# Optimization experiments

Hardware: AMD Instinct MI355X
Metric: run time of the kernel (lower is better)

## Reference

```python
import jax, jax.numpy as jnp
import numpy as np

EMBED = 1024
HEADS = 16
HEAD_DIM = EMBED // HEADS


def setup_inputs() -> dict:
    key = jax.random.key(0)
    ks = jax.random.split(key, 8)
    N, S = 4, 2048
    scale = 1.0 / np.sqrt(HEAD_DIM)
    return {
        "values": jax.random.normal(ks[0], (N, S, EMBED), jnp.float32),
        "keys": jax.random.normal(ks[1], (N, S, EMBED), jnp.float32),
        "query": jax.random.normal(ks[2], (N, S, EMBED), jnp.float32),
        "Wv": jax.random.normal(ks[3], (HEAD_DIM, HEAD_DIM), jnp.float32) * scale,
        "Wk": jax.random.normal(ks[4], (HEAD_DIM, HEAD_DIM), jnp.float32) * scale,
        "Wq": jax.random.normal(ks[5], (HEAD_DIM, HEAD_DIM), jnp.float32) * scale,
        "Wo": jax.random.normal(ks[6], (EMBED, EMBED), jnp.float32) / np.sqrt(EMBED),
        "bo": jax.random.normal(ks[7], (EMBED,), jnp.float32) * 0.01,
    }


def reference(values, keys, query, Wv, Wk, Wq, Wo, bo):
    N = query.shape[0]
    # reshape to [N, S, H, D]
    v = values.reshape(N, -1, HEADS, HEAD_DIM)
    k = keys.reshape(N, -1, HEADS, HEAD_DIM)
    q = query.reshape(N, -1, HEADS, HEAD_DIM)
    # per-head linear projections (torch Linear: x @ W.T)
    v = jnp.einsum("nshd,ed->nshe", v, Wv)
    k = jnp.einsum("nshd,ed->nshe", k, Wk)
    q = jnp.einsum("nshd,ed->nshe", q, Wq)
    # full attention matrix [N, H, Q, K]; note scale uses embed_size**0.5 as in source
    energy = jnp.einsum("nqhd,nkhd->nhqk", q, k)
    attn = jax.nn.softmax(energy / jnp.sqrt(jnp.asarray(EMBED, energy.dtype)), axis=3)
    out = jnp.einsum("nhql,nlhd->nqhd", attn, v).reshape(N, -1, EMBED)
    return out @ Wo.T + bo
```

## Files before the change

### kernel.cpp

```cpp
#include <hip/hip_runtime.h>
#include <hip/hip_bf16.h>

#define EMBED 1024
#define HEADS 16
#define HD    64
#define NB    4
#define SEQ   2048

typedef __bf16 bf16x2 __attribute__((ext_vector_type(2)));
typedef __bf16 bf16x8 __attribute__((ext_vector_type(8)));
typedef float  f32x4  __attribute__((ext_vector_type(4)));
typedef float  f32x16 __attribute__((ext_vector_type(16)));

__device__ __forceinline__ unsigned short f2bf(float f) {
    union { float f; unsigned u; } v; v.f = f;
    unsigned r = v.u + 0x7fffu + ((v.u >> 16) & 1u);
    return (unsigned short)(r >> 16);
}
__device__ __forceinline__ unsigned pack2(float a, float b) {
#if __has_builtin(__builtin_amdgcn_cvt_pk_bf16_f32)
    union { bf16x2 v; unsigned u; } c;
    c.v = __builtin_amdgcn_cvt_pk_bf16_f32(a, b);
    return c.u;
#else
    return (unsigned)f2bf(a) | ((unsigned)f2bf(b) << 16);
#endif
}

__global__ __launch_bounds__(256) void cvt_kernel(const float* __restrict__ src,
                                                  unsigned* __restrict__ dst) {
    int i = blockIdx.x * 256 + threadIdx.x;
    float4 v = ((const float4*)src)[i];
    uint2 o;
    o.x = pack2(v.x, v.y);
    o.y = pack2(v.z, v.w);
    ((uint2*)dst)[i] = o;
}

__global__ __launch_bounds__(256) void proj_kernel(
    const float* __restrict__ xq, const float* __restrict__ xk, const float* __restrict__ xv,
    const float* __restrict__ Wq, const float* __restrict__ Wk, const float* __restrict__ Wv,
    unsigned short* __restrict__ Qp, unsigned short* __restrict__ Kp, unsigned short* __restrict__ Vt)
{
    __shared__ __align__(16) unsigned short Wl[64 * 72];
    __shared__ __align__(16) unsigned short Xl[256 * 72];

    int bx = blockIdx.x;
    int p  = bx >> 9;
    int r  = bx & 511;
    int st = r & 7, h = (r >> 3) & 15, n = r >> 7;
    int s0 = st * 256;

    const float* x = (p == 0) ? xq : (p == 1) ? xk : xv;
    const float* W = (p == 0) ? Wq : (p == 1) ? Wk : Wv;
    const float sc = (p == 0) ? 0.045084220027780106f : 1.0f;

    int tid = threadIdx.x;

    for (int i = 0; i < 4; ++i) {
        int idx = tid + i * 256;
        int row = idx >> 4, c4 = idx & 15;
        float4 wv = ((const float4*)W)[row * 16 + c4];
        uint2 pw;
        pw.x = pack2(wv.x, wv.y);
        pw.y = pack2(wv.z, wv.w);
        *(uint2*)&Wl[row * 72 + c4 * 4] = pw;
    }
    const float* xbase = x + (size_t)(n * SEQ + s0) * EMBED + h * HD;
    for (int i = 0; i < 16; ++i) {
        int idx = tid + i * 256;
        int row = idx >> 4, c4 = idx & 15;
        float4 v = *(const float4*)(xbase + (size_t)row * EMBED + c4 * 4);
        uint2 px;
        px.x = pack2(v.x, v.y);
        px.y = pack2(v.z, v.w);
        *(uint2*)&Xl[row * 72 + c4 * 4] = px;
    }
    __syncthreads();

    int w = tid >> 6, lane = tid & 63, ln = lane & 15, qd = lane >> 4;

    bf16x8 a[4][2], b[4][2];
#pragma unroll
    for (int mt = 0; mt < 4; ++mt)
#pragma unroll
        for (int kt = 0; kt < 2; ++kt)
            a[mt][kt] = *(const bf16x8*)&Xl[(w * 64 + mt * 16 + ln) * 72 + kt * 32 + qd * 8];
#pragma unroll
    for (int i = 0; i < 4; ++i)
#pragma unroll
        for (int kt = 0; kt < 2; ++kt)
            b[i][kt] = *(const bf16x8*)&Wl[(i * 16 + ln) * 72 + kt * 32 + qd * 8];

    f32x4 acc[4][4];
    const f32x4 fz = {0.f, 0.f, 0.f, 0.f};
#pragma unroll
    for (int i = 0; i < 4; ++i)
#pragma unroll
        for (int j = 0; j < 4; ++j) acc[i][j] = fz;

    if (p < 2) {
#pragma unroll
        for (int i = 0; i < 4; ++i)
#pragma unroll
            for (int j = 0; j < 4; ++j) {
                acc[i][j] = __builtin_amdgcn_mfma_f32_16x16x32_bf16(b[i][0], a[j][0], acc[i][j], 0, 0, 0);
                acc[i][j] = __builtin_amdgcn_mfma_f32_16x16x32_bf16(b[i][1], a[j][1], acc[i][j], 0, 0, 0);
            }
#pragma unroll
        for (int i = 0; i < 4; ++i)
#pragma unroll
            for (int j = 0; j < 4; ++j) {
                uint2 pk;
                pk.x = pack2(acc[i][j][0] * sc, acc[i][j][1] * sc);
                pk.y = pack2(acc[i][j][2] * sc, acc[i][j][3] * sc);
                *(uint2*)&Xl[(w * 64 + j * 16 + ln) * 72 + i * 16 + qd * 4] = pk;
            }
        __syncthreads();
        unsigned short* outp = (p == 0 ? Qp : Kp) + (size_t)(n * HEADS + h) * SEQ * HD + (size_t)s0 * HD;
        for (int i = 0; i < 8; ++i) {
            int idx = tid + i * 256;
            int row = idx >> 3, ch = idx & 7;
            *(uint4*)(outp + (size_t)row * HD + ch * 8) = *(const uint4*)&Xl[row * 72 + ch * 8];
        }
    } else {
#pragma unroll
        for (int mt = 0; mt < 4; ++mt)
#pragma unroll
            for (int i = 0; i < 4; ++i) {
                acc[mt][i] = __builtin_amdgcn_mfma_f32_16x16x32_bf16(a[mt][0], b[i][0], acc[mt][i], 0, 0, 0);
                acc[mt][i] = __builtin_amdgcn_mfma_f32_16x16x32_bf16(a[mt][1], b[i][1], acc[mt][i], 0, 0, 0);
            }
        __syncthreads();
#pragma unroll
        for (int mt = 0; mt < 4; ++mt)
#pragma unroll
            for (int i = 0; i < 4; ++i) {
                uint2 pk;
                pk.x = pack2(acc[mt][i][0], acc[mt][i][1]);
                pk.y = pack2(acc[mt][i][2], acc[mt][i][3]);
                *(uint2*)&Xl[(i * 16 + ln) * 264 + w * 64 + mt * 16 + qd * 4] = pk;
            }
        __syncthreads();
        unsigned short* outp = Vt + (size_t)(n * HEADS + h) * HD * SEQ + s0;
        for (int i = 0; i < 8; ++i) {
            int idx = tid + i * 256;
            int row = idx >> 5, ch = idx & 31;
            *(uint4*)(outp + (size_t)row * SEQ + ch * 8) = *(const uint4*)&Xl[row * 264 + ch * 8];
        }
    }
}

__global__ __launch_bounds__(512, 4) void attn_kernel(
    const unsigned short* __restrict__ Qp, const unsigned short* __restrict__ Kp,
    const unsigned short* __restrict__ Vt, unsigned short* __restrict__ Xattn)
{
    __shared__ __align__(16) unsigned short SMEM[18432];
    unsigned short* Kl = SMEM;
    unsigned short* Vl = SMEM + 9216;

    int bx = blockIdx.x;
    int head = bx >> 3, qt = bx & 7;
    int n = head >> 4, h16 = head & 15;
    int q0 = qt * 256;

    int tid = threadIdx.x;
    int w = tid >> 6, lane = tid & 63;
    int qc = lane & 31, hh = lane >> 5;

    const unsigned short* Qb = Qp + (size_t)head * SEQ * HD;
    const unsigned short* Kb = Kp + (size_t)head * SEQ * HD;
    const unsigned short* Vb = Vt + (size_t)head * HD * SEQ;

    bf16x8 qb[4];
    {
        int qrow = q0 + w * 32 + qc;
#pragma unroll
        for (int kk = 0; kk < 4; ++kk)
            qb[kk] = *(const bf16x8*)(Qb + (size_t)qrow * HD + kk * 16 + hh * 8);
    }

    f32x16 ot0, ot1;
#pragma unroll
    for (int i = 0; i < 16; ++i) { ot0[i] = 0.f; ot1[i] = 0.f; }
    float lsum = 0.f;

    int srow = tid >> 3, sch = tid & 7;

    uint4 rK, rV;
    rK = *(const uint4*)(Kb + (size_t)srow * HD + sch * 8);
    rV = *(const uint4*)(Vb + (size_t)srow * SEQ + 0 + sch * 8);
    *(uint4*)&Kl[srow * 72 + sch * 8] = rK;
    *(uint4*)&Vl[srow * 72 + sch * 8] = rV;
    rK = *(const uint4*)(Kb + (size_t)(64 + srow) * HD + sch * 8);
    rV = *(const uint4*)(Vb + (size_t)srow * SEQ + 64 + sch * 8);

    for (int kc = 0; kc < SEQ; kc += 64) {
        int cur = (kc >> 6) & 1, nxt = cur ^ 1;
        int curo = cur * 4608;
        __syncthreads();

        if (kc + 64 < SEQ) {
            *(uint4*)&Kl[nxt * 4608 + srow * 72 + sch * 8] = rK;
            *(uint4*)&Vl[nxt * 4608 + srow * 72 + sch * 8] = rV;
            int kn = kc + 128 <= SEQ - 64 ? kc + 128 : SEQ - 64;
            rK = *(const uint4*)(Kb + (size_t)(kn + srow) * HD + sch * 8);
            rV = *(const uint4*)(Vb + (size_t)srow * SEQ + kn + sch * 8);
        }

        unsigned pk[2][8];
#pragma unroll
        for (int kt = 0; kt < 2; ++kt) {
            f32x16 c;
#pragma unroll
            for (int i = 0; i < 16; ++i) c[i] = 0.f;
#pragma unroll
            for (int kk = 0; kk < 4; ++kk) {
                bf16x8 ka = *(const bf16x8*)&Kl[curo + (kt * 32 + qc) * 72 + kk * 16 + hh * 8];
                c = __builtin_amdgcn_mfma_f32_32x32x16_bf16(ka, qb[kk], c, 0, 0, 0);
            }
#pragma unroll
            for (int i = 0; i < 8; ++i) {
                float p0 = __builtin_amdgcn_exp2f(c[2 * i]);
                float p1 = __builtin_amdgcn_exp2f(c[2 * i + 1]);
                lsum += p0 + p1;
                pk[kt][i] = pack2(p0, p1);
            }
        }

#pragma unroll
        for (int g = 0; g < 4; ++g) {
            const unsigned* P = pk[g >> 1];
            int base = (g & 1) * 4;
            unsigned s0 = hh ? P[base + 0] : P[base + 2];
            unsigned s1 = hh ? P[base + 1] : P[base + 3];
            unsigned r0 = (unsigned)__shfl_xor((int)s0, 32);
            unsigned r1 = (unsigned)__shfl_xor((int)s1, 32);
            union { unsigned u[4]; bf16x8 v; } bb;
            bb.u[0] = hh ? r0 : P[base + 0];
            bb.u[1] = hh ? r1 : P[base + 1];
            bb.u[2] = hh ? P[base + 2] : r0;
            bb.u[3] = hh ? P[base + 3] : r1;
            bf16x8 va0 = *(const bf16x8*)&Vl[curo + qc * 72 + g * 16 + hh * 8];
            bf16x8 va1 = *(const bf16x8*)&Vl[curo + (32 + qc) * 72 + g * 16 + hh * 8];
            ot0 = __builtin_amdgcn_mfma_f32_32x32x16_bf16(va0, bb.v, ot0, 0, 0, 0);
            ot1 = __builtin_amdgcn_mfma_f32_32x32x16_bf16(va1, bb.v, ot1, 0, 0, 0);
        }
    }

    lsum += __shfl_xor(lsum, 32);
    float inv = 1.0f / lsum;

    __syncthreads();
    int qlocal = w * 32 + qc;
#pragma unroll
    for (int dt = 0; dt < 2; ++dt) {
        const f32x16& o = dt ? ot1 : ot0;
#pragma unroll
        for (int g = 0; g < 4; ++g) {
            uint2 p;
            p.x = pack2(o[4 * g + 0] * inv, o[4 * g + 1] * inv);
            p.y = pack2(o[4 * g + 2] * inv, o[4 * g + 3] * inv);
            *(uint2*)&SMEM[qlocal * 72 + dt * 32 + g * 8 + hh * 4] = p;
        }
    }
    __syncthreads();
    unsigned short* ob = Xattn + (size_t)(n * SEQ + q0) * EMBED + h16 * HD;
#pragma unroll
    for (int i = 0; i < 4; ++i) {
        int idx = tid + i * 512;
        int row = idx >> 3, ch = idx & 7;
        *(uint4*)(ob + (size_t)row * EMBED + ch * 8) = *(const uint4*)&SMEM[row * 72 + ch * 8];
    }
}

__global__ __launch_bounds__(256) void outproj_kernel(
    const unsigned short* __restrict__ X, const unsigned short* __restrict__ Wb,
    const float* __restrict__ bo, float* __restrict__ out)
{
    __shared__ __align__(16) unsigned short Al[128 * 72];
    __shared__ __align__(16) unsigned short Bl[128 * 72];

    int bx = blockIdx.x;
    int cm = bx >> 3, cn = bx & 7;
    int m0 = cm * 128, c0 = cn * 128;
    int tid = threadIdx.x;
    int w = tid >> 6, lane = tid & 63, ln = lane & 15, qd = lane >> 4;
    int rh = (w & 1) * 64, chh = (w >> 1) * 64;

    f32x4 acc[4][4];
    const f32x4 fz = {0.f, 0.f, 0.f, 0.f};
#pragma unroll
    for (int mt = 0; mt < 4; ++mt)
#pragma unroll
        for (int nt = 0; nt < 4; ++nt) acc[mt][nt] = fz;

    for (int k0 = 0; k0 < EMBED; k0 += 64) {
        for (int i = 0; i < 4; ++i) {
            int idx = tid + i * 256;
            int row = idx >> 3, ch = idx & 7;
            uint4 av = *(const uint4*)(X  + (size_t)(m0 + row) * EMBED + k0 + ch * 8);
            uint4 bv = *(const uint4*)(Wb + (size_t)(c0 + row) * EMBED + k0 + ch * 8);
            *(uint4*)&Al[row * 72 + ch * 8] = av;
            *(uint4*)&Bl[row * 72 + ch * 8] = bv;
        }
        __syncthreads();
        bf16x8 af[4][2], bf_[4][2];
#pragma unroll
        for (int mt = 0; mt < 4; ++mt)
#pragma unroll
            for (int kt = 0; kt < 2; ++kt)
                af[mt][kt] = *(const bf16x8*)&Al[(rh + mt * 16 + ln) * 72 + kt * 32 + qd * 8];
#pragma unroll
        for (int nt = 0; nt < 4; ++nt)
#pragma unroll
            for (int kt = 0; kt < 2; ++kt)
                bf_[nt][kt] = *(const bf16x8*)&Bl[(chh + nt * 16 + ln) * 72 + kt * 32 + qd * 8];
#pragma unroll
        for (int mt = 0; mt < 4; ++mt)
#pragma unroll
            for (int nt = 0; nt < 4; ++nt) {
                acc[mt][nt] = __builtin_amdgcn_mfma_f32_16x16x32_bf16(af[mt][0], bf_[nt][0], acc[mt][nt], 0, 0, 0);
                acc[mt][nt] = __builtin_amdgcn_mfma_f32_16x16x32_bf16(af[mt][1], bf_[nt][1], acc[mt][nt], 0, 0, 0);
            }
        __syncthreads();
    }

#pragma unroll
    for (int nt = 0; nt < 4; ++nt) {
        int col = c0 + chh + nt * 16 + ln;
        float bias = bo[col];
#pragma unroll
        for (int mt = 0; mt < 4; ++mt) {
            int row = m0 + rh + mt * 16 + qd * 4;
#pragma unroll
            for (int rg = 0; rg < 4; ++rg)
                out[(size_t)(row + rg) * EMBED + col] = acc[mt][nt][rg] + bias;
        }
    }
}

extern "C" void kernel_launch(void* const* d_in, const int* in_sizes, int n_in,
                              void* d_out, int out_size, void* d_ws, size_t ws_size,
                              hipStream_t stream) {
    const float* values = (const float*)d_in[0];
    const float* keys   = (const float*)d_in[1];
    const float* query  = (const float*)d_in[2];
    const float* Wv     = (const float*)d_in[3];
    const float* Wk     = (const float*)d_in[4];
    const float* Wq     = (const float*)d_in[5];
    const float* Wo     = (const float*)d_in[6];
    const float* bo     = (const float*)d_in[7];
    float* out = (float*)d_out;

    unsigned short* ws = (unsigned short*)d_ws;
    const size_t HSZ = (size_t)NB * HEADS * SEQ * HD;
    unsigned short* Qp = ws;
    unsigned short* Kp = Qp + HSZ;
    unsigned short* Vt = Kp + HSZ;
    unsigned short* Xa = Vt + HSZ;
    unsigned short* Wb = Xa + HSZ;

    cvt_kernel<<<1024, 256, 0, stream>>>(Wo, (unsigned*)Wb);
    proj_kernel<<<1536, 256, 0, stream>>>(query, keys, values, Wq, Wk, Wv, Qp, Kp, Vt);
    attn_kernel<<<512, 512, 0, stream>>>(Qp, Kp, Vt, Xa);
    outproj_kernel<<<512, 256, 0, stream>>>(Xa, Wb, bo, out);
}
```

Baseline: 276.5 us.

## Prefetch output-projection tiles into registers and use permlane32 swap in attention

```diff
diff --git a/kernel.cpp b/kernel.cpp
--- a/kernel.cpp
+++ b/kernel.cpp
@@ -11,6 +11,7 @@
 typedef __bf16 bf16x8 __attribute__((ext_vector_type(8)));
 typedef float  f32x4  __attribute__((ext_vector_type(4)));
 typedef float  f32x16 __attribute__((ext_vector_type(16)));
+typedef unsigned uint2v __attribute__((ext_vector_type(2)));
 
 __device__ __forceinline__ unsigned short f2bf(float f) {
     union { float f; unsigned u; } v; v.f = f;
@@ -183,7 +184,7 @@
     f32x16 ot0, ot1;
 #pragma unroll
     for (int i = 0; i < 16; ++i) { ot0[i] = 0.f; ot1[i] = 0.f; }
-    float lsum = 0.f;
+    float ls[4] = {0.f, 0.f, 0.f, 0.f};
 
     int srow = tid >> 3, sch = tid & 7;
 
@@ -223,7 +224,7 @@
             for (int i = 0; i < 8; ++i) {
                 float p0 = __builtin_amdgcn_exp2f(c[2 * i]);
                 float p1 = __builtin_amdgcn_exp2f(c[2 * i + 1]);
-                lsum += p0 + p1;
+                ls[i & 3] += p0 + p1;
                 pk[kt][i] = pack2(p0, p1);
             }
         }
@@ -232,15 +233,24 @@
         for (int g = 0; g < 4; ++g) {
             const unsigned* P = pk[g >> 1];
             int base = (g & 1) * 4;
+            union { unsigned u[4]; bf16x8 v; } bb;
+#if __has_builtin(__builtin_amdgcn_permlane32_swap)
+            uint2v r  = __builtin_amdgcn_permlane32_swap(P[base + 0], P[base + 2], false, false);
+            uint2v rr = __builtin_amdgcn_permlane32_swap(P[base + 1], P[base + 3], false, false);
+            bb.u[0] = r.x;
+            bb.u[1] = rr.x;
+            bb.u[2] = r.y;
+            bb.u[3] = rr.y;
+#else
             unsigned s0 = hh ? P[base + 0] : P[base + 2];
             unsigned s1 = hh ? P[base + 1] : P[base + 3];
             unsigned r0 = (unsigned)__shfl_xor((int)s0, 32);
             unsigned r1 = (unsigned)__shfl_xor((int)s1, 32);
-            union { unsigned u[4]; bf16x8 v; } bb;
             bb.u[0] = hh ? r0 : P[base + 0];
             bb.u[1] = hh ? r1 : P[base + 1];
             bb.u[2] = hh ? P[base + 2] : r0;
             bb.u[3] = hh ? P[base + 3] : r1;
+#endif
             bf16x8 va0 = *(const bf16x8*)&Vl[curo + qc * 72 + g * 16 + hh * 8];
             bf16x8 va1 = *(const bf16x8*)&Vl[curo + (32 + qc) * 72 + g * 16 + hh * 8];
             ot0 = __builtin_amdgcn_mfma_f32_32x32x16_bf16(va0, bb.v, ot0, 0, 0, 0);
@@ -248,6 +258,7 @@
         }
     }
 
+    float lsum = (ls[0] + ls[1]) + (ls[2] + ls[3]);
     lsum += __shfl_xor(lsum, 32);
     float inv = 1.0f / lsum;
 
@@ -295,16 +306,32 @@
 #pragma unroll
         for (int nt = 0; nt < 4; ++nt) acc[mt][nt] = fz;
 
+    int srow = tid >> 1, sch = tid & 1;
+
+    uint4 rA[4], rB[4];
+#pragma unroll
+    for (int i = 0; i < 4; ++i) {
+        rA[i] = *(const uint4*)(X  + (size_t)(m0 + srow) * EMBED + (sch * 4 + i) * 8);
+        rB[i] = *(const uint4*)(Wb + (size_t)(c0 + srow) * EMBED + (sch * 4 + i) * 8);
+    }
+
     for (int k0 = 0; k0 < EMBED; k0 += 64) {
+#pragma unroll
         for (int i = 0; i < 4; ++i) {
-            int idx = tid + i * 256;
-            int row = idx >> 3, ch = idx & 7;
-            uint4 av = *(const uint4*)(X  + (size_t)(m0 + row) * EMBED + k0 + ch * 8);
-            uint4 bv = *(const uint4*)(Wb + (size_t)(c0 + row) * EMBED + k0 + ch * 8);
-            *(uint4*)&Al[row * 72 + ch * 8] = av;
-            *(uint4*)&Bl[row * 72 + ch * 8] = bv;
-        }
-        __syncthreads();
+            *(uint4*)&Al[srow * 72 + (sch * 4 + i) * 8] = rA[i];
+            *(uint4*)&Bl[srow * 72 + (sch * 4 + i) * 8] = rB[i];
+        }
+        __syncthreads();
+
+        if (k0 + 64 < EMBED) {
+            int kn = k0 + 64;
+#pragma unroll
+            for (int i = 0; i < 4; ++i) {
+                rA[i] = *(const uint4*)(X  + (size_t)(m0 + srow) * EMBED + kn + (sch * 4 + i) * 8);
+                rB[i] = *(const uint4*)(Wb + (size_t)(c0 + srow) * EMBED + kn + (sch * 4 + i) * 8);
+            }
+        }
+
         bf16x8 af[4][2], bf_[4][2];
 #pragma unroll
         for (int mt = 0; mt < 4; ++mt)
```

Measured after the change: 330.5 us. 1.2x slower.
